# Optimization experiments

Hardware: AMD Instinct MI355X
Metric: run time of the kernel (lower is better)

The kernel has to match this reference:

```python
import jax, jax.numpy as jnp
import numpy as np

NUM_BINS_X = 512
NUM_BINS_Y = 512
XL, YL, XH, YH = 0.0, 0.0, 1.0, 1.0
ROUTING_H = 50000.0
ROUTING_V = 50000.0
MACRO_UTIL_H = 10.0
MACRO_UTIL_V = 10.0
NUM_NETS = 131072
PINS_PER_NET = 4
NUM_MOVABLE = 50000
NUM_TERMINALS = 5000
NUM_NODES = NUM_MOVABLE + NUM_TERMINALS
NUM_PINS = NUM_NETS * PINS_PER_NET
BIN_SIZE_X = (XH - XL) / NUM_BINS_X
BIN_SIZE_Y = (YH - YL) / NUM_BINS_Y


def setup_inputs():
    key = jax.random.key(0)
    k1, k2, k3, k4 = jax.random.split(key, 4)
    # pin_pos = [x_0..x_P-1, y_0..y_P-1], pos = [x_0..x_N-1, y_0..y_N-1]
    pin_pos = jax.random.uniform(k1, (2 * NUM_PINS,), dtype=jnp.float32, minval=XL, maxval=XH)
    pos = jax.random.uniform(k2, (2 * NUM_NODES,), dtype=jnp.float32, minval=XL, maxval=0.9 * (XH - XL))
    node_size_x = jax.random.uniform(k3, (NUM_NODES,), dtype=jnp.float32, minval=0.01, maxval=0.05)
    node_size_y = jax.random.uniform(k4, (NUM_NODES,), dtype=jnp.float32, minval=0.01, maxval=0.05)
    net_weights = jnp.ones((NUM_NETS,), jnp.float32)
    rng = np.random.default_rng(0)
    flat_netpin = jnp.asarray(rng.permutation(NUM_PINS).astype(np.int32))
    movable = rng.choice(NUM_MOVABLE, 64, replace=False)
    fixed = NUM_MOVABLE + rng.choice(NUM_TERMINALS, 32, replace=False)
    macro_indexes = jnp.asarray(np.concatenate([movable, fixed]).astype(np.int32))
    return dict(pos=pos, pin_pos=pin_pos, node_size_x=node_size_x, node_size_y=node_size_y,
                net_weights=net_weights, flat_netpin=flat_netpin, macro_indexes=macro_indexes)


def _bin_overlap(lo, hi, origin, bin_size, num_bins):
    # [N, num_bins]: overlap length of interval [lo, hi] with each bin along one axis
    edges = origin + bin_size * jnp.arange(num_bins, dtype=lo.dtype)
    return jnp.clip(jnp.minimum(hi[:, None], edges[None, :] + bin_size)
                    - jnp.maximum(lo[:, None], edges[None, :]), 0.0, None)


def _blur3(m, sigma):
    # torchvision GaussianBlur(kernel_size=3, sigma), separable, reflect padding
    x = jnp.array([-1.0, 0.0, 1.0], m.dtype)
    k = jnp.exp(-0.5 * (x / sigma) ** 2)
    k = k / k.sum()
    mp = jnp.pad(m, ((1, 1), (0, 0)), mode='reflect')
    m = k[0] * mp[:-2] + k[1] * mp[1:-1] + k[2] * mp[2:]
    mp = jnp.pad(m, ((0, 0), (1, 1)), mode='reflect')
    return k[0] * mp[:, :-2] + k[1] * mp[:, 1:-1] + k[2] * mp[:, 2:]


def _rudy_maps(pos, pin_pos, node_size_x, node_size_y, net_weights, flat_netpin, macro_indexes):
    # net bounding boxes from pins (fixed PINS_PER_NET pins per net)
    px = pin_pos[:NUM_PINS][flat_netpin].reshape(NUM_NETS, PINS_PER_NET)
    py = pin_pos[NUM_PINS:][flat_netpin].reshape(NUM_NETS, PINS_PER_NET)
    x_min, x_max = px.min(1), px.max(1)
    y_min, y_max = py.min(1), py.max(1)
    ox = _bin_overlap(x_min, x_max, XL, BIN_SIZE_X, NUM_BINS_X)   # [N, Bx]
    oy = _bin_overlap(y_min, y_max, YL, BIN_SIZE_Y, NUM_BINS_Y)   # [N, By]
    wh = net_weights / (y_max - y_min)  # RUDY horizontal demand density
    wv = net_weights / (x_max - x_min)  # RUDY vertical demand density
    H = jnp.einsum('nx,ny->xy', ox * wh[:, None], oy)
    V = jnp.einsum('nx,ny->xy', ox * wv[:, None], oy)
    # macro contributions
    mx = pos[macro_indexes]
    my = pos[NUM_NODES + macro_indexes]
    msx = node_size_x[macro_indexes]
    msy = node_size_y[macro_indexes]
    area = msx * msy
    mox = _bin_overlap(mx, mx + msx, XL, BIN_SIZE_X, NUM_BINS_X)
    moy = _bin_overlap(my, my + msy, YL, BIN_SIZE_Y, NUM_BINS_Y)
    H = H + jnp.einsum('mx,my->xy', mox * (MACRO_UTIL_H / area)[:, None], moy)
    V = V + jnp.einsum('mx,my->xy', mox * (MACRO_UTIL_V / area)[:, None], moy)
    num_bins = NUM_BINS_X * NUM_BINS_Y
    H = H / (ROUTING_H / num_bins)
    V = V / (ROUTING_V / num_bins)
    sigma = min((XH - XL) / BIN_SIZE_X, (YH - YL) / BIN_SIZE_Y) / 16.0
    return _blur3(H, sigma), _blur3(V, sigma)


def reference(pos, pin_pos, node_size_x, node_size_y, net_weights, flat_netpin, macro_indexes):
    H, V = _rudy_maps(pos, pin_pos, node_size_x, node_size_y, net_weights, flat_netpin, macro_indexes)
    h_ov = jnp.maximum(H - 1.0, 0.0)
    v_ov = jnp.maximum(V - 1.0, 0.0)
    h_cnt = (h_ov > 0).sum()
    v_cnt = (v_ov > 0).sum()
    total_overflow = h_cnt + v_cnt          # total overflow bin area
    max_overflow = jnp.maximum(h_cnt, v_cnt)  # jit-compatible proxy for largest contour area
    route_utilization_map = jnp.maximum(jnp.abs(H), jnp.abs(V))
    return route_utilization_map, max_overflow, total_overflow
```

## Files before the change

kernel.cpp:

```cpp
#include <hip/hip_runtime.h>

#define N_NETS  131072
#define N_PINS  (N_NETS * 4)
#define N_NODES 55000
#define NBBLK   256
#define RPB     516
#define NPARTS  4
#define CELLCAP 96

__device__ uint4 g_ent[64 * NBBLK * CELLCAP * 2];
__device__ unsigned short g_cellcnt[64 * NBBLK];
__device__ float g_part[NPARTS * 512 * 1024];
__device__ int      g_cnt2[2];
__device__ unsigned g_tick;

__global__ __launch_bounds__(512) void k_bbox(
    const float* __restrict__ pos, const float* __restrict__ pin_pos,
    const float* __restrict__ nsx, const float* __restrict__ nsy,
    const float* __restrict__ nw,  const int* __restrict__ fnp,
    const int* __restrict__ mid, int nm)
{
    __shared__ int s_cnt[64];
    int tid = threadIdx.x;
    int b = blockIdx.x;
    if (b == 0 && tid == 0) { g_cnt2[0] = 0; g_cnt2[1] = 0; g_tick = 0; }
    if (tid < 64) s_cnt[tid] = 0;
    __syncthreads();

    int tEnd = min((b + 1) * RPB, N_NETS + nm);
    for (int t = b * RPB + tid; t < tEnd; t += 512) {
        float xmin, xmax, ymin, ymax, wh, wv;
        if (t < N_NETS) {
            int4 p = ((const int4*)fnp)[t];
            float x0 = pin_pos[p.x], x1 = pin_pos[p.y], x2 = pin_pos[p.z], x3 = pin_pos[p.w];
            float y0 = pin_pos[N_PINS + p.x], y1 = pin_pos[N_PINS + p.y];
            float y2 = pin_pos[N_PINS + p.z], y3 = pin_pos[N_PINS + p.w];
            xmin = fminf(fminf(x0, x1), fminf(x2, x3));
            xmax = fmaxf(fmaxf(x0, x1), fmaxf(x2, x3));
            ymin = fminf(fminf(y0, y1), fminf(y2, y3));
            ymax = fmaxf(fmaxf(y0, y1), fmaxf(y2, y3));
            float w = nw[t];
            wh = w / (ymax - ymin);
            wv = w / (xmax - xmin);
        } else {
            int idx = mid[t - N_NETS];
            xmin = pos[idx]; ymin = pos[N_NODES + idx];
            float sx = nsx[idx], sy = nsy[idx];
            xmax = xmin + sx; ymax = ymin + sy;
            wh = wv = 10.0f / (sx * sy);
        }
        const float B = 1.0f / 512.0f;
        int xl = min(max((int)(xmin * 512.0f), 0), 511);
        int xh = min(max((int)(xmax * 512.0f), 0), 511);
        int yl = min(max((int)(ymin * 512.0f), 0), 511);
        int yh = min(max((int)(ymax * 512.0f), 0), 511);
        unsigned w0c = (unsigned)yl | ((unsigned)(yl + 1) << 16);
        unsigned w1c = (unsigned)yh | ((unsigned)(yh + 1) << 16);
        uint4 Bq = make_uint4(__float_as_uint((yl + 1) * B - ymin),
                              __float_as_uint(ymin - yl * B),
                              __float_as_uint(ymax - (yh + 1) * B),
                              __float_as_uint(yh * B - ymax));

        auto put = [&](int row, float px) {
            int s = row & 63;
            int slot = atomicAdd(&s_cnt[s], 1);
            if (slot < CELLCAP) {
                uint4 A;
                A.x = w0c | ((unsigned)(row >> 6) << 29);
                A.y = w1c;
                A.z = __float_as_uint(px * wh);
                A.w = __float_as_uint(px * wv);
                unsigned base = ((unsigned)(s * NBBLK + b) * CELLCAP + (unsigned)slot) * 2u;
                g_ent[base]     = A;
                g_ent[base + 1] = Bq;
            }
        };
        put(xl, (xl + 1) * B - xmin);
        if (xl + 1 < 512) put(xl + 1, xmin - xl * B);
        put(xh, xmax - (xh + 1) * B);
        if (xh + 1 < 512) put(xh + 1, xh * B - xmax);
    }
    __syncthreads();
    if (tid < 64) g_cellcnt[tid * NBBLK + b] = (unsigned short)min(s_cnt[tid], CELLCAP);
}

__global__ __launch_bounds__(1024) void k_deposit() {
    __shared__ float tile[8706];
    __shared__ int s_pref[64];
    __shared__ int s_total;
    int tid = threadIdx.x;
    int s = blockIdx.x >> 2, p = blockIdx.x & 3;
#pragma unroll
    for (int k = tid; k < 8706; k += 1024) tile[k] = 0.0f;

    int lob = p * 64;
    if (tid < 64) {
        int c = (int)g_cellcnt[s * NBBLK + lob + tid];
        int v = c;
#pragma unroll
        for (int off = 1; off < 64; off <<= 1) {
            int tv = __shfl_up(v, off);
            if (tid >= off) v += tv;
        }
        s_pref[tid] = v - c;
        if (tid == 63) s_total = v;
    }
    __syncthreads();

    int total = s_total;
    for (int k = tid; k < total; k += 1024) {
        int loJ = 0, hiJ = 63;
#pragma unroll
        for (int st = 0; st < 6; ++st) {
            int mid_ = (loJ + hiJ + 1) >> 1;
            if (s_pref[mid_] <= k) loJ = mid_; else hiJ = mid_ - 1;
        }
        unsigned gidx = ((unsigned)(s * NBBLK + lob + loJ) * CELLCAP
                         + (unsigned)(k - s_pref[loJ])) * 2u;
        uint4 A  = g_ent[gidx];
        uint4 Bq = g_ent[gidx + 1];
        int rr = (int)(A.x >> 29);
        unsigned c0 = A.x & 0xFFFFu, c1 = (A.x >> 16) & 0x1FFFu;
        unsigned c2 = A.y & 0xFFFFu, c3 = A.y >> 16;
        float ah = __uint_as_float(A.z), av = __uint_as_float(A.w);
        float p0 = __uint_as_float(Bq.x), p1 = __uint_as_float(Bq.y);
        float p2 = __uint_as_float(Bq.z), p3 = __uint_as_float(Bq.w);
        int base = rr * 1024;
        int i0 = (c0 < 512u) ? base + 2 * (int)c0 : 8192;
        int i1 = (c1 < 512u) ? base + 2 * (int)c1 : 8192;
        int i2 = (c2 < 512u) ? base + 2 * (int)c2 : 8192;
        int i3 = (c3 < 512u) ? base + 2 * (int)c3 : 8192;
        unsafeAtomicAdd(&tile[i0],     ah * p0);
        unsafeAtomicAdd(&tile[i0 + 1], av * p0);
        unsafeAtomicAdd(&tile[i1],     ah * p1);
        unsafeAtomicAdd(&tile[i1 + 1], av * p1);
        unsafeAtomicAdd(&tile[i2],     ah * p2);
        unsafeAtomicAdd(&tile[i2 + 1], av * p2);
        unsafeAtomicAdd(&tile[i3],     ah * p3);
        unsafeAtomicAdd(&tile[i3 + 1], av * p3);
    }
    __syncthreads();

    int wid = tid >> 6, lane = tid & 63;
    if (wid < 8) {
        float2* rowp = (float2*)&tile[wid * 1024];
        float cx = 0.0f, cy = 0.0f;
        for (int ch = 0; ch < 8; ++ch) {
            float2 v = rowp[ch * 64 + lane];
#pragma unroll
            for (int off = 1; off < 64; off <<= 1) {
                float tx = __shfl_up(v.x, off);
                float ty = __shfl_up(v.y, off);
                if (lane >= off) { v.x += tx; v.y += ty; }
            }
            v.x += cx; v.y += cy;
            rowp[ch * 64 + lane] = v;
            cx = __shfl(v.x, 63); cy = __shfl(v.y, 63);
        }
    }
    __syncthreads();
    int dstp = p * 524288 + (s << 10);
#pragma unroll
    for (int k = 0; k < 8; ++k) {
        int idx = tid + k * 1024;
        int rr = idx >> 10, cc = idx & 1023;
        g_part[dstp + (rr << 16) + cc] = tile[idx];
    }
}

__global__ __launch_bounds__(1024) void k_finish(float* __restrict__ out) {
    __shared__ float sB[16 * 512];
    __shared__ int scnt[2];
    int tid = threadIdx.x;
    int b = blockIdx.x;
    int lane = tid & 63;
    int c20 = tid & 31;
    int xg = tid >> 5;
    int jj = (c20 < 10) ? c20 : c20 - 10;
    int cy = 8 * b - 1 + jj;
    if (cy < 0) cy = 1;
    if (cy > 511) cy = 510;
    int map = (c20 < 10) ? 0 : 1;
    int gcol = 2 * cy + map;
    const float kw  = expf(-0.5f / 1024.0f);
    const float k1n = 1.0f / (1.0f + 2.0f * kw);
    const float k0n = kw * k1n;
    const float scale = 262144.0f / 50000.0f;
    bool active = c20 < 20;
    int t8  = (c20 < 10) ? c20 - 1 : c20 - 11;

    for (int xo4 = 0; xo4 < 4; ++xo4) {
        float acc[4];
#pragma unroll
        for (int j = 0; j < 4; ++j) {
            int x = (xo4 * 4 + j) * 32 + xg;
            float v = 0.0f;
            if (active) {
                int base = x * 1024 + gcol;
#pragma unroll
                for (int p = 0; p < NPARTS; ++p) v += g_part[p * 524288 + base];
            }
            acc[j] = v;
        }
#pragma unroll
        for (int j = 0; j < 4; ++j) {
            int x = (xo4 * 4 + j) * 32 + xg;
            float vm = __shfl(acc[j], lane - 1);
            float vp = __shfl(acc[j], lane + 1);
            float yb = (k0n * (vm + vp) + k1n * acc[j]) * scale;
            if (t8 >= 0 && t8 < 8) sB[(map * 8 + t8) * 512 + x] = yb;
        }
    }
    __syncthreads();

    {
        int w = tid >> 6;
        float carry = 0.0f;
        for (int ch = 0; ch < 8; ++ch) {
            float v = sB[w * 512 + ch * 64 + lane];
#pragma unroll
            for (int off = 1; off < 64; off <<= 1) {
                float tv = __shfl_up(v, off);
                if (lane >= off) v += tv;
            }
            v += carry;
            sB[w * 512 + ch * 64 + lane] = v;
            carry = __shfl(v, 63);
        }
    }
    __syncthreads();

    int x = tid >> 1, qh = (tid & 1) * 4;
    int xm = (x == 0) ? 1 : x - 1;
    int xp = (x == 511) ? 510 : x + 1;
    float4 o;
    int ch_ = 0, cv_ = 0;
#pragma unroll
    for (int k = 0; k < 4; ++k) {
        int tt = qh + k;
        const float* rH = &sB[tt * 512];
        const float* rV = &sB[(8 + tt) * 512];
        float hv = k0n * (rH[xm] + rH[xp]) + k1n * rH[x];
        float vv = k0n * (rV[xm] + rV[xp]) + k1n * rV[x];
        ((float*)&o)[k] = fmaxf(fabsf(hv), fabsf(vv));
        ch_ += (hv > 1.0f); cv_ += (vv > 1.0f);
    }
    *(float4*)&out[x * 512 + 8 * b + qh] = o;
#pragma unroll
    for (int off = 32; off > 0; off >>= 1) {
        ch_ += __shfl_down(ch_, off);
        cv_ += __shfl_down(cv_, off);
    }
    if (tid < 2) scnt[tid] = 0;
    __syncthreads();
    if (lane == 0) { atomicAdd(&scnt[0], ch_); atomicAdd(&scnt[1], cv_); }
    __syncthreads();
    if (tid == 0) {
        atomicAdd(&g_cnt2[0], scnt[0]);
        atomicAdd(&g_cnt2[1], scnt[1]);
        __threadfence();
        unsigned old = atomicAdd(&g_tick, 1u);
        if ((old & 63u) == 63u) {
            __threadfence();
            int h = atomicAdd(&g_cnt2[0], 0);
            int v = atomicAdd(&g_cnt2[1], 0);
            out[262144] = (float)((h > v) ? h : v);
            out[262145] = (float)(h + v);
        }
    }
}

extern "C" void kernel_launch(void* const* d_in, const int* in_sizes, int n_in,
                              void* d_out, int out_size, void* d_ws, size_t ws_size,
                              hipStream_t stream) {
    const float* pos     = (const float*)d_in[0];
    const float* pin_pos = (const float*)d_in[1];
    const float* nsx     = (const float*)d_in[2];
    const float* nsy     = (const float*)d_in[3];
    const float* nw      = (const float*)d_in[4];
    const int*   fnp     = (const int*)d_in[5];
    const int*   mid     = (const int*)d_in[6];
    int nm = in_sizes[6];
    float* out = (float*)d_out;

    hipLaunchKernelGGL(k_bbox,    dim3(NBBLK), dim3(512), 0, stream,
                       pos, pin_pos, nsx, nsy, nw, fnp, mid, nm);
    hipLaunchKernelGGL(k_deposit, dim3(256), dim3(1024), 0, stream);
    hipLaunchKernelGGL(k_finish,  dim3(64), dim3(1024), 0, stream, out);
}
```

Before: 65.27 us.

## Bucket rows contiguously, halve partials, and transpose partial layout for coalesced finish reads

Rows are now grouped into slabs of eight consecutive rows (row>>3) instead of strided modulo-64 groups. Each deposit block merges two halves of the bbox blocks (NPARTS 4 to 2, CELLCAP 96 to 128) and writes its tile transposed as float4 chunks into a [part][map][y][x] layout. The finish kernel then reads coalesced along x and applies the y-direction blur with direct neighbour loads instead of shuffles. This cuts partial-buffer traffic and the number of partial sums, but gives fewer deposit blocks (128) with more entries each, and a higher per-cell capacity that could still overflow.

New measurement: 118.3 us. 1.81x slower.

```diff
diff --git a/kernel.cpp b/kernel.cpp
--- a/kernel.cpp
+++ b/kernel.cpp
@@ -5,12 +5,12 @@
 #define N_NODES 55000
 #define NBBLK   256
 #define RPB     516
-#define NPARTS  4
-#define CELLCAP 96
+#define NPARTS  2
+#define CELLCAP 128
 
 __device__ uint4 g_ent[64 * NBBLK * CELLCAP * 2];
 __device__ unsigned short g_cellcnt[64 * NBBLK];
-__device__ float g_part[NPARTS * 512 * 1024];
+__device__ float g_part[NPARTS * 2 * 512 * 512];
 __device__ int      g_cnt2[2];
 __device__ unsigned g_tick;
 
@@ -62,11 +62,11 @@
                               __float_as_uint(yh * B - ymax));
 
         auto put = [&](int row, float px) {
-            int s = row & 63;
+            int s = row >> 3;
             int slot = atomicAdd(&s_cnt[s], 1);
             if (slot < CELLCAP) {
                 uint4 A;
-                A.x = w0c | ((unsigned)(row >> 6) << 29);
+                A.x = w0c | ((unsigned)(row & 7) << 29);
                 A.y = w1c;
                 A.z = __float_as_uint(px * wh);
                 A.w = __float_as_uint(px * wv);
@@ -86,32 +86,36 @@
 
 __global__ __launch_bounds__(1024) void k_deposit() {
     __shared__ float tile[8706];
-    __shared__ int s_pref[64];
+    __shared__ int s_pref[128];
+    __shared__ int s_wt[2];
     __shared__ int s_total;
     int tid = threadIdx.x;
-    int s = blockIdx.x >> 2, p = blockIdx.x & 3;
+    int s = blockIdx.x >> 1, p = blockIdx.x & 1;
 #pragma unroll
     for (int k = tid; k < 8706; k += 1024) tile[k] = 0.0f;
 
-    int lob = p * 64;
-    if (tid < 64) {
+    int lob = p * 128;
+    if (tid < 128) {
         int c = (int)g_cellcnt[s * NBBLK + lob + tid];
         int v = c;
 #pragma unroll
         for (int off = 1; off < 64; off <<= 1) {
             int tv = __shfl_up(v, off);
-            if (tid >= off) v += tv;
+            if ((tid & 63) >= off) v += tv;
         }
         s_pref[tid] = v - c;
-        if (tid == 63) s_total = v;
-    }
+        if ((tid & 63) == 63) s_wt[tid >> 6] = v;
+    }
+    __syncthreads();
+    if (tid >= 64 && tid < 128) s_pref[tid] += s_wt[0];
+    if (tid == 0) s_total = s_wt[0] + s_wt[1];
     __syncthreads();
 
     int total = s_total;
     for (int k = tid; k < total; k += 1024) {
-        int loJ = 0, hiJ = 63;
-#pragma unroll
-        for (int st = 0; st < 6; ++st) {
+        int loJ = 0, hiJ = 127;
+#pragma unroll
+        for (int st = 0; st < 7; ++st) {
             int mid_ = (loJ + hiJ + 1) >> 1;
             if (s_pref[mid_] <= k) loJ = mid_; else hiJ = mid_ - 1;
         }
@@ -159,12 +163,17 @@
         }
     }
     __syncthreads();
-    int dstp = p * 524288 + (s << 10);
-#pragma unroll
-    for (int k = 0; k < 8; ++k) {
-        int idx = tid + k * 1024;
-        int rr = idx >> 10, cc = idx & 1023;
-        g_part[dstp + (rr << 16) + cc] = tile[idx];
+
+    {
+        int c = tid;
+        int mp = c & 1, cy = c >> 1;
+        float t0 = tile[c],            t1 = tile[c + 1024];
+        float t2 = tile[c + 2048],     t3 = tile[c + 3072];
+        float t4 = tile[c + 4096],     t5 = tile[c + 5120];
+        float t6 = tile[c + 6144],     t7 = tile[c + 7168];
+        float* dst = &g_part[(((p * 2 + mp) * 512 + cy) << 9) + 8 * s];
+        *(float4*)dst       = make_float4(t0, t1, t2, t3);
+        *(float4*)(dst + 4) = make_float4(t4, t5, t6, t7);
     }
 }
 
@@ -174,42 +183,27 @@
     int tid = threadIdx.x;
     int b = blockIdx.x;
     int lane = tid & 63;
-    int c20 = tid & 31;
-    int xg = tid >> 5;
-    int jj = (c20 < 10) ? c20 : c20 - 10;
-    int cy = 8 * b - 1 + jj;
-    if (cy < 0) cy = 1;
-    if (cy > 511) cy = 510;
-    int map = (c20 < 10) ? 0 : 1;
-    int gcol = 2 * cy + map;
     const float kw  = expf(-0.5f / 1024.0f);
     const float k1n = 1.0f / (1.0f + 2.0f * kw);
     const float k0n = kw * k1n;
     const float scale = 262144.0f / 50000.0f;
-    bool active = c20 < 20;
-    int t8  = (c20 < 10) ? c20 - 1 : c20 - 11;
-
-    for (int xo4 = 0; xo4 < 4; ++xo4) {
-        float acc[4];
-#pragma unroll
-        for (int j = 0; j < 4; ++j) {
-            int x = (xo4 * 4 + j) * 32 + xg;
-            float v = 0.0f;
-            if (active) {
-                int base = x * 1024 + gcol;
-#pragma unroll
-                for (int p = 0; p < NPARTS; ++p) v += g_part[p * 524288 + base];
-            }
-            acc[j] = v;
-        }
-#pragma unroll
-        for (int j = 0; j < 4; ++j) {
-            int x = (xo4 * 4 + j) * 32 + xg;
-            float vm = __shfl(acc[j], lane - 1);
-            float vp = __shfl(acc[j], lane + 1);
-            float yb = (k0n * (vm + vp) + k1n * acc[j]) * scale;
-            if (t8 >= 0 && t8 < 8) sB[(map * 8 + t8) * 512 + x] = yb;
-        }
+
+#pragma unroll
+    for (int k = 0; k < 8; ++k) {
+        int i = tid + k * 1024;
+        int x = i & 511, r = i >> 9;
+        int mp = r >> 3, t = r & 7;
+        int cy = 8 * b + t;
+        int cym = (cy == 0) ? 1 : cy - 1;
+        int cyp = (cy == 511) ? 510 : cy + 1;
+        float v = 0.0f;
+#pragma unroll
+        for (int p = 0; p < NPARTS; ++p) {
+            const float* g = &g_part[((p * 2 + mp) * 512) << 9];
+            v += k0n * (g[(cym << 9) + x] + g[(cyp << 9) + x])
+               + k1n * g[(cy << 9) + x];
+        }
+        sB[r * 512 + x] = v * scale;
     }
     __syncthreads();
 
@@ -285,6 +279,6 @@
 
     hipLaunchKernelGGL(k_bbox,    dim3(NBBLK), dim3(512), 0, stream,
                        pos, pin_pos, nsx, nsy, nw, fnp, mid, nm);
-    hipLaunchKernelGGL(k_deposit, dim3(256), dim3(1024), 0, stream);
+    hipLaunchKernelGGL(k_deposit, dim3(128), dim3(1024), 0, stream);
     hipLaunchKernelGGL(k_finish,  dim3(64), dim3(1024), 0, stream, out);
 }
```
